# Performance work log

Hardware: AMD Instinct MI355X
Metric: run time of the kernel (lower is better)

Reference implementation:

```python
import jax, jax.numpy as jnp
import numpy as np

K = 7
TAU = 0.1
ANCHORS = 512
CANDIDATES = 2048
B, C, H, W = 16, 384, 96, 96
RADIUS = K // 2
K2 = K * K

_dy, _dx = np.meshgrid(np.arange(-RADIUS, RADIUS + 1), np.arange(-RADIUS, RADIUS + 1), indexing='ij')
OFF_Y = jnp.asarray(_dy.reshape(-1).astype(np.int32))  # [K2]
OFF_X = jnp.asarray(_dx.reshape(-1).astype(np.int32))  # [K2]


def _normalize(x):
    # F.normalize(x, dim=1): L2 over channel dim, eps=1e-12
    n = jnp.sqrt(jnp.sum(x * x, axis=1, keepdims=True))
    return x / jnp.maximum(n, 1e-12)


def _local_sims_shared(feat, anchors_yx):
    # feat [B,C,H,W], anchors_yx [M,2] shared across batch -> [B,M,K2]
    ys, xs = anchors_yx[:, 0], anchors_yx[:, 1]          # [M]
    yy = ys[:, None] + OFF_Y[None, :]                    # [M,K2]
    xx = xs[:, None] + OFF_X[None, :]                    # [M,K2]
    center = feat[:, :, ys, xs]                          # [B,C,M]
    neigh = feat[:, :, yy, xx]                           # [B,C,M,K2]
    return jnp.einsum('bcm,bcmk->bmk', center, neigh)


def _local_sims_per_image(feat, anchors_byx):
    # feat [B,C,H,W], anchors_byx [Bm,M,2] per-image anchors -> [B,M,K2]
    b, c, h, w = feat.shape
    flat = feat.reshape(b, c, h * w)
    ys, xs = anchors_byx[..., 0], anchors_byx[..., 1]    # [B,M]
    lin_c = ys * w + xs                                  # [B,M]
    lin_n = (ys[..., None] + OFF_Y) * w + (xs[..., None] + OFF_X)  # [B,M,K2]
    gather = jax.vmap(lambda f, idx: f[:, idx])          # f [C,HW], idx [...]
    center = gather(flat, lin_c)                         # [B,C,M]
    neigh = gather(flat, lin_n)                          # [B,C,M,K2]
    return jnp.einsum('bcm,bcmk->bmk', center, neigh)


def setup_inputs() -> dict:
    key = jax.random.key(0)
    k1, k2, k3, k4 = jax.random.split(key, 4)
    student = jax.random.normal(k1, (B, C, H, W), dtype=jnp.float32)
    teacher = jax.random.normal(k2, (B, C, H, W), dtype=jnp.float32)
    # anchors valid region: [radius, H-radius-1] x [radius, W-radius-1]
    ys = jax.random.randint(k3, (CANDIDATES,), RADIUS, H - RADIUS, dtype=jnp.int32)
    xs = jax.random.randint(k4, (CANDIDATES,), RADIUS, W - RADIUS, dtype=jnp.int32)
    candidate_anchors = jnp.stack([ys, xs], axis=1)      # [Mc,2]
    return {"student": student, "teacher": teacher, "candidate_anchors": candidate_anchors}


def reference(student, teacher, candidate_anchors):
    t_norm = _normalize(teacher)
    # --- teacher-entropy based anchor selection (no_grad in original) ---
    sim_cand = _local_sims_shared(t_norm, candidate_anchors) / TAU   # [B,Mc,K2]
    p = jax.nn.softmax(sim_cand, axis=2)
    ent = -jnp.sum(p * jnp.log(p + 1e-6), axis=2)                    # [B,Mc]
    # per_image=True, kcenter_top_m=0 -> lowest-entropy top-k per image
    _, sel_idx = jax.lax.top_k(-ent, ANCHORS)                        # [B,A]
    anchors = candidate_anchors[sel_idx]                             # [B,A,2]
    # --- local affinity KL ---
    s_norm = _normalize(student)
    sim_s = _local_sims_per_image(s_norm, anchors) / TAU             # [B,A,K2]
    sim_t = _local_sims_per_image(t_norm, anchors) / TAU
    log_ps = jax.nn.log_softmax(sim_s, axis=2)
    log_pt = jax.nn.log_softmax(sim_t, axis=2)
    pt = jnp.exp(log_pt)
    # F.kl_div(log_ps, pt, 'none').sum(2).mean()
    loss = jnp.mean(jnp.sum(pt * (log_pt - log_ps), axis=2))
    return loss
```

## Files before the change

### kernel.cpp

```cpp
#include <hip/hip_runtime.h>
#include <math.h>

#define B 16
#define C 384
#define CPAD 385
#define H 96
#define W 96
#define HW (H*W)
#define M 2048
#define K2 49
#define RAD 3
#define NSEL 512
#define INV_TAU 10.0f
#define TP 32

__device__ inline float wave_max(float v){
  #pragma unroll
  for (int o = 32; o; o >>= 1) v = fmaxf(v, __shfl_xor(v, o));
  return v;
}
__device__ inline float wave_sum(float v){
  #pragma unroll
  for (int o = 32; o; o >>= 1) v += __shfl_xor(v, o);
  return v;
}

__device__ inline float dot_wave(float2 c0, float2 c1, float2 c2,
                                 const float2* __restrict__ nb2){
  float2 n0 = nb2[0], n1 = nb2[64], n2 = nb2[128];
  float acc = c0.x * n0.x;
  acc = fmaf(c0.y, n0.y, acc);
  acc = fmaf(c1.x, n1.x, acc); acc = fmaf(c1.y, n1.y, acc);
  acc = fmaf(c2.x, n2.x, acc); acc = fmaf(c2.y, n2.y, acc);
  acc += __shfl_xor(acc, 32); acc += __shfl_xor(acc, 16);
  acc += __shfl_xor(acc, 8);  acc += __shfl_xor(acc, 4);
  acc += __shfl_xor(acc, 2);  acc += __shfl_xor(acc, 1);
  return acc;
}


__global__ void tnorm_kernel(const float* __restrict__ src, float* __restrict__ dst){
  int blk = blockIdx.x;
  int b = blk / (HW / TP);
  int pixbase = (blk % (HW / TP)) * TP;
  __shared__ float tile[TP][CPAD];
  __shared__ float scale[TP];
  const float* sb = src + (size_t)b * C * HW + pixbase;
  int tx = threadIdx.x & 31;
  int ty = threadIdx.x >> 5;
  #pragma unroll 4
  for (int c0 = 0; c0 < C; c0 += 8){
    tile[tx][c0 + ty] = sb[(size_t)(c0 + ty) * HW + tx];
  }
  __syncthreads();
  int pix = threadIdx.x >> 3;
  int j = threadIdx.x & 7;
  float ss = 0.f;
  #pragma unroll 4
  for (int c = j * 48; c < j * 48 + 48; ++c){ float v = tile[pix][c]; ss = fmaf(v, v, ss); }
  ss += __shfl_xor(ss, 1); ss += __shfl_xor(ss, 2); ss += __shfl_xor(ss, 4);
  if (j == 0) scale[pix] = 1.0f / fmaxf(sqrtf(ss), 1e-12f);
  __syncthreads();
  float4* db4 = (float4*)(dst + ((size_t)b * HW + pixbase) * C);
  #pragma unroll 4
  for (int l = threadIdx.x; l < TP * (C / 4); l += 256){
    int p = l / (C / 4), c4 = l - p * (C / 4);
    float s = scale[p];
    float4 v;
    v.x = tile[p][c4 * 4 + 0] * s;
    v.y = tile[p][c4 * 4 + 1] * s;
    v.z = tile[p][c4 * 4 + 2] * s;
    v.w = tile[p][c4 * 4 + 3] * s;
    db4[(size_t)p * (C / 4) + c4] = v;
  }
}

__global__ __launch_bounds__(256) void cand2_kernel(const float* __restrict__ fT,
                             const int* __restrict__ anch,
                             float* __restrict__ simc, float* __restrict__ ent){
  int bm = blockIdx.x * 4 + (threadIdx.x >> 6);
  int b = bm >> 11, m = bm & (M - 1);
  int lane = threadIdx.x & 63;
  int ay = anch[2 * m], ax = anch[2 * m + 1];
  const float* img = fT + (size_t)b * HW * C;
  const float2* ctr2 = (const float2*)(img + (size_t)(ay * W + ax) * C) + lane;
  float2 c0 = ctr2[0], c1 = ctr2[64], c2 = ctr2[128];
  float mysim = 0.f;
  int k = 0;
  for (int dy = -RAD; dy <= RAD; ++dy){
    const float* rowp = img + (size_t)((ay + dy) * W + (ax - RAD)) * C;
    #pragma unroll
    for (int dx = 0; dx < 7; ++dx){
      const float2* nb2 = (const float2*)(rowp + (size_t)dx * C) + lane;
      float acc = dot_wave(c0, c1, c2, nb2);
      if (lane == k) mysim = acc;
      ++k;
    }
  }
  mysim *= INV_TAU;
  float v = (lane < K2) ? mysim : -INFINITY;
  float mx = wave_max(v);
  float e = (lane < K2) ? expf(mysim - mx) : 0.f;
  float se = wave_sum(e);
  float p = e / se;
  float term = (lane < K2) ? (-p * logf(p + 1e-6f)) : 0.f;
  float en = wave_sum(term);
  if (lane == 0) ent[bm] = en;
  if (lane < K2) simc[(size_t)bm * K2 + lane] = mysim;
}

__global__ void select_kernel(const float* __restrict__ ent, int* __restrict__ sel){
  int blk = blockIdx.x;
  int b = blk >> 3;
  int i = (blk & 7) * 256 + threadIdx.x;
  __shared__ float se[M];
  for (int j = threadIdx.x; j < M; j += 256) se[j] = ent[b * M + j];
  __syncthreads();
  float ei = se[i];
  int r = 0;
  for (int j = 0; j < M; ++j){
    float ej = se[j];
    r += (ej < ei) || (ej == ei && j < i);
  }
  if (r < NSEL) sel[b * NSEL + r] = i;
}

__global__ __launch_bounds__(256) void kl2_kernel(const float* __restrict__ fS,
                           const int* __restrict__ anch,
                           const float* __restrict__ simc, const int* __restrict__ sel,
                           float* __restrict__ klpart){
  int bj = blockIdx.x * 4 + (threadIdx.x >> 6);
  int b = bj >> 9, j = bj & (NSEL - 1);
  int lane = threadIdx.x & 63;
  int m = sel[b * NSEL + j];
  int ay = anch[2 * m], ax = anch[2 * m + 1];
  const float* img = fS + (size_t)b * HW * C;
  const float2* ctr2 = (const float2*)(img + (size_t)(ay * W + ax) * C) + lane;
  float2 c0 = ctr2[0], c1 = ctr2[64], c2 = ctr2[128];
  float mysim = 0.f;
  int k = 0;
  for (int dy = -RAD; dy <= RAD; ++dy){
    const float* rowp = img + (size_t)((ay + dy) * W + (ax - RAD)) * C;
    #pragma unroll
    for (int dx = 0; dx < 7; ++dx){
      const float2* nb2 = (const float2*)(rowp + (size_t)dx * C) + lane;
      float acc = dot_wave(c0, c1, c2, nb2);
      if (lane == k) mysim = acc;
      ++k;
    }
  }
  float sim_sv = mysim * INV_TAU;
  float sim_tv = (lane < K2) ? simc[((size_t)b * M + m) * K2 + lane] : -INFINITY;

  float vs = (lane < K2) ? sim_sv : -INFINITY;
  float mxs = wave_max(vs);
  float es = (lane < K2) ? expf(sim_sv - mxs) : 0.f;
  float sums = wave_sum(es);
  float ls = sim_sv - mxs - logf(sums);

  float mxt = wave_max(sim_tv);
  float et = (lane < K2) ? expf(sim_tv - mxt) : 0.f;
  float sumt = wave_sum(et);
  float lt = sim_tv - mxt - logf(sumt);

  float pt = et / sumt;
  float term = (lane < K2) ? pt * (lt - ls) : 0.f;
  float kl = wave_sum(term);
  if (lane == 0) klpart[bj] = kl;
}

__global__ void reduce_kernel(const float* __restrict__ part, float* __restrict__ out){
  float s = 0.f;
  for (int i = threadIdx.x; i < B * NSEL; i += 256) s += part[i];
  s = wave_sum(s);
  __shared__ float wsum[4];
  if ((threadIdx.x & 63) == 0) wsum[threadIdx.x >> 6] = s;
  __syncthreads();
  if (threadIdx.x == 0) out[0] = (wsum[0] + wsum[1] + wsum[2] + wsum[3]) * (1.0f / (B * NSEL));
}


__global__ void norms_kernel(const float* __restrict__ t, const float* __restrict__ s,
                             float* __restrict__ inv_t, float* __restrict__ inv_s){
  int pix = blockIdx.x * blockDim.x + threadIdx.x;
  if (pix >= B * HW) return;
  int b = pix / HW, p = pix - b * HW;
  const float* tb = t + (size_t)b * C * HW + p;
  const float* sb = s + (size_t)b * C * HW + p;
  float at = 0.f, as = 0.f;
  #pragma unroll 4
  for (int c = 0; c < C; ++c){
    float v = tb[(size_t)c * HW]; at = fmaf(v, v, at);
    float u = sb[(size_t)c * HW]; as = fmaf(u, u, as);
  }
  inv_t[pix] = 1.0f / fmaxf(sqrtf(at), 1e-12f);
  inv_s[pix] = 1.0f / fmaxf(sqrtf(as), 1e-12f);
}

__global__ void cand_kernel(const float* __restrict__ t, const int* __restrict__ anch,
                            const float* __restrict__ inv_t,
                            float* __restrict__ simc, float* __restrict__ ent){
  int bm = blockIdx.x;
  int b = bm >> 11, m = bm & (M - 1);
  int lane = threadIdx.x;
  int ay = anch[2 * m], ax = anch[2 * m + 1];
  int k = lane < K2 ? lane : 0;
  int dy = k / 7 - RAD, dx = k - (k / 7) * 7 - RAD;
  int pc = ay * W + ax;
  int pk = (ay + dy) * W + (ax + dx);
  const float* base = t + (size_t)b * C * HW;
  float acc = 0.f;
  #pragma unroll 4
  for (int c = 0; c < C; ++c){
    const float* row = base + (size_t)c * HW;
    acc = fmaf(row[pc], row[pk], acc);
  }
  float sim = acc * inv_t[b * HW + pc] * inv_t[b * HW + pk] * INV_TAU;
  float v = (lane < K2) ? sim : -INFINITY;
  float mx = wave_max(v);
  float e = (lane < K2) ? expf(sim - mx) : 0.f;
  float se = wave_sum(e);
  float p = e / se;
  float term = (lane < K2) ? (-p * logf(p + 1e-6f)) : 0.f;
  float en = wave_sum(term);
  if (lane == 0) ent[bm] = en;
  if (lane < K2) simc[(size_t)bm * K2 + lane] = sim;
}

__global__ void kl_kernel(const float* __restrict__ s, const int* __restrict__ anch,
                          const float* __restrict__ inv_s, const float* __restrict__ simc,
                          const int* __restrict__ sel, float* __restrict__ klpart){
  int bj = blockIdx.x;
  int b = bj >> 9, j = bj & (NSEL - 1);
  int lane = threadIdx.x;
  int m = sel[b * NSEL + j];
  int ay = anch[2 * m], ax = anch[2 * m + 1];
  int k = lane < K2 ? lane : 0;
  int dy = k / 7 - RAD, dx = k - (k / 7) * 7 - RAD;
  int pc = ay * W + ax;
  int pk = (ay + dy) * W + (ax + dx);
  const float* base = s + (size_t)b * C * HW;
  float acc = 0.f;
  #pragma unroll 4
  for (int c = 0; c < C; ++c){
    const float* row = base + (size_t)c * HW;
    acc = fmaf(row[pc], row[pk], acc);
  }
  float sim_sv = acc * inv_s[b * HW + pc] * inv_s[b * HW + pk] * INV_TAU;
  float sim_tv = (lane < K2) ? simc[((size_t)b * M + m) * K2 + lane] : -INFINITY;

  float vs = (lane < K2) ? sim_sv : -INFINITY;
  float mxs = wave_max(vs);
  float es = (lane < K2) ? expf(sim_sv - mxs) : 0.f;
  float sums = wave_sum(es);
  float ls = sim_sv - mxs - logf(sums);

  float mxt = wave_max(sim_tv);
  float et = (lane < K2) ? expf(sim_tv - mxt) : 0.f;
  float sumt = wave_sum(et);
  float lt = sim_tv - mxt - logf(sumt);

  float pt = et / sumt;
  float term = (lane < K2) ? pt * (lt - ls) : 0.f;
  float kl = wave_sum(term);
  if (lane == 0) klpart[bj] = kl;
}

extern "C" void kernel_launch(void* const* d_in, const int* in_sizes, int n_in,
                              void* d_out, int out_size, void* d_ws, size_t ws_size,
                              hipStream_t stream){
  const float* student = (const float*)d_in[0];
  const float* teacher = (const float*)d_in[1];
  const int*   anch    = (const int*)d_in[2];
  float* out = (float*)d_out;

  const size_t fbuf_elems = (size_t)B * HW * C;
  const size_t simc_elems = (size_t)B * M * K2;
  size_t req = (fbuf_elems + simc_elems + (size_t)B * M + (size_t)B * NSEL) * sizeof(float)
             + (size_t)B * NSEL * sizeof(int);

  if (ws_size >= req){
    float* fbuf   = (float*)d_ws;
    float* simc   = fbuf + fbuf_elems;
    float* ent    = simc + simc_elems;
    float* klpart = ent + (size_t)B * M;
    int*   sel    = (int*)(klpart + (size_t)B * NSEL);

    hipLaunchKernelGGL(tnorm_kernel, dim3(B * (HW / TP)), dim3(256), 0, stream, teacher, fbuf);
    hipLaunchKernelGGL(cand2_kernel, dim3(B * M / 4), dim3(256), 0, stream, fbuf, anch, simc, ent);
    hipLaunchKernelGGL(select_kernel, dim3(B * 8), dim3(256), 0, stream, ent, sel);
    hipLaunchKernelGGL(tnorm_kernel, dim3(B * (HW / TP)), dim3(256), 0, stream, student, fbuf);
    hipLaunchKernelGGL(kl2_kernel, dim3(B * NSEL / 4), dim3(256), 0, stream, fbuf, anch, simc, sel, klpart);
    hipLaunchKernelGGL(reduce_kernel, dim3(1), dim3(256), 0, stream, klpart, out);
  } else {
    float* ws2    = (float*)d_ws;
    float* inv_t  = ws2;
    float* inv_s  = inv_t + B * HW;
    float* ent    = inv_s + B * HW;
    float* simc   = ent + B * M;
    float* klpart = simc + simc_elems;
    int*   sel    = (int*)(klpart + (size_t)B * NSEL);

    hipLaunchKernelGGL(norms_kernel, dim3((B * HW + 255) / 256), dim3(256), 0, stream,
                       teacher, student, inv_t, inv_s);
    hipLaunchKernelGGL(cand_kernel, dim3(B * M), dim3(64), 0, stream,
                       teacher, anch, inv_t, simc, ent);
    hipLaunchKernelGGL(select_kernel, dim3(B * 8), dim3(256), 0, stream, ent, sel);
    hipLaunchKernelGGL(kl_kernel, dim3(B * NSEL), dim3(64), 0, stream,
                       student, anch, inv_s, simc, sel, klpart);
    hipLaunchKernelGGL(reduce_kernel, dim3(1), dim3(256), 0, stream, klpart, out);
  }
}
```

Baseline: 907.7 us.

## Rework patch dot products into 4-neighbor wave groups, sort anchors spatially, swizzle blocks

Each wave now splits into four 16-lane groups, so one pass computes four neighbor dot products with 12 float2 loads per lane, double-buffered under scheduling barriers. This replaces 49 full-wave reductions with 14 shorter ones. Candidate anchors are sorted by 8x8 spatial tile in a new kernel, and block ids are swizzled so nearby anchors run together for better L2 reuse. Launch bounds now request 4 blocks per CU. The risks are higher register pressure and a small extra sort kernel.

```diff
diff --git a/kernel.cpp b/kernel.cpp
--- a/kernel.cpp
+++ b/kernel.cpp
@@ -25,17 +25,48 @@
   return v;
 }
 
-__device__ inline float dot_wave(float2 c0, float2 c1, float2 c2,
-                                 const float2* __restrict__ nb2){
-  float2 n0 = nb2[0], n1 = nb2[64], n2 = nb2[128];
-  float acc = c0.x * n0.x;
-  acc = fmaf(c0.y, n0.y, acc);
-  acc = fmaf(c1.x, n1.x, acc); acc = fmaf(c1.y, n1.y, acc);
-  acc = fmaf(c2.x, n2.x, acc); acc = fmaf(c2.y, n2.y, acc);
-  acc += __shfl_xor(acc, 32); acc += __shfl_xor(acc, 16);
-  acc += __shfl_xor(acc, 8);  acc += __shfl_xor(acc, 4);
-  acc += __shfl_xor(acc, 2);  acc += __shfl_xor(acc, 1);
-  return acc;
+__device__ __forceinline__ float patch_sims(const float* __restrict__ img,
+                                            int ay, int ax, int lane){
+  int g = lane >> 4, t = lane & 15;
+  const float2* cp = (const float2*)(img + (size_t)(ay * W + ax) * C) + t;
+  float2 c[12];
+  #pragma unroll
+  for (int j = 0; j < 12; ++j) c[j] = cp[16 * j];
+  float mysim = 0.f;
+  float2 bA[12], bB[12];
+
+#define PLOAD(buf, pp) { \
+    int dxl = ((pp) & 1) * 4 + g; if (dxl > 6) dxl = 6; \
+    const float2* np = (const float2*)(img + \
+        (size_t)((ay + ((pp) >> 1) - RAD) * W + (ax - RAD + dxl)) * C) + t; \
+    _Pragma("unroll") for (int j = 0; j < 12; ++j) buf[j] = np[16 * j]; }
+
+#define PCOMP(buf, pp) { \
+    float a0 = 0.f, a1 = 0.f; \
+    _Pragma("unroll") for (int j = 0; j < 6; ++j){ \
+      a0 = fmaf(c[j].x, buf[j].x, a0); a0 = fmaf(c[j].y, buf[j].y, a0); \
+      a1 = fmaf(c[j+6].x, buf[j+6].x, a1); a1 = fmaf(c[j+6].y, buf[j+6].y, a1); } \
+    float a = a0 + a1; \
+    a += __shfl_xor(a, 8); a += __shfl_xor(a, 4); \
+    a += __shfl_xor(a, 2); a += __shfl_xor(a, 1); \
+    int kbase = ((pp) >> 1) * 7 + ((pp) & 1) * 4; \
+    int npass = ((pp) & 1) ? 3 : 4; \
+    float v = __shfl(a, ((lane - kbase) & 3) << 4); \
+    if (lane >= kbase && lane < kbase + npass) mysim = v; }
+
+  PLOAD(bA, 0);
+  #pragma unroll
+  for (int pp = 0; pp < 14; pp += 2){
+    PLOAD(bB, pp + 1);
+    __builtin_amdgcn_sched_barrier(0);
+    PCOMP(bA, pp);
+    if (pp + 2 < 14) PLOAD(bA, pp + 2);
+    __builtin_amdgcn_sched_barrier(0);
+    PCOMP(bB, pp + 1);
+  }
+#undef PLOAD
+#undef PCOMP
+  return mysim;
 }
 
 
@@ -75,29 +106,35 @@
   }
 }
 
-__global__ __launch_bounds__(256) void cand2_kernel(const float* __restrict__ fT,
-                             const int* __restrict__ anch,
+__global__ void sort_kernel(const int* __restrict__ anch, int* __restrict__ order){
+  int i = blockIdx.x * 256 + threadIdx.x;
+  __shared__ int keys[M];
+  for (int j = threadIdx.x; j < M; j += 256){
+    int ay = anch[2 * j], ax = anch[2 * j + 1];
+    keys[j] = (((ay >> 3) * 12 + (ax >> 3)) << 11) + j;
+  }
+  __syncthreads();
+  int ki = keys[i];
+  int r = 0;
+  #pragma unroll 4
+  for (int j = 0; j < M; ++j) r += (keys[j] < ki) ? 1 : 0;
+  order[r] = i;
+}
+
+__global__ __launch_bounds__(256, 4) void cand2_kernel(const float* __restrict__ fT,
+                             const int* __restrict__ anch, const int* __restrict__ order,
                              float* __restrict__ simc, float* __restrict__ ent){
-  int bm = blockIdx.x * 4 + (threadIdx.x >> 6);
-  int b = bm >> 11, m = bm & (M - 1);
+  int nwg = B * M / 4;
+  int bid = blockIdx.x;
+  int swz = (bid & 7) * (nwg >> 3) + (bid >> 3);
+  int bm = swz * 4 + (threadIdx.x >> 6);
+  int b = bm >> 11, mi = bm & (M - 1);
   int lane = threadIdx.x & 63;
+  int m = order ? order[mi] : mi;
   int ay = anch[2 * m], ax = anch[2 * m + 1];
   const float* img = fT + (size_t)b * HW * C;
-  const float2* ctr2 = (const float2*)(img + (size_t)(ay * W + ax) * C) + lane;
-  float2 c0 = ctr2[0], c1 = ctr2[64], c2 = ctr2[128];
-  float mysim = 0.f;
-  int k = 0;
-  for (int dy = -RAD; dy <= RAD; ++dy){
-    const float* rowp = img + (size_t)((ay + dy) * W + (ax - RAD)) * C;
-    #pragma unroll
-    for (int dx = 0; dx < 7; ++dx){
-      const float2* nb2 = (const float2*)(rowp + (size_t)dx * C) + lane;
-      float acc = dot_wave(c0, c1, c2, nb2);
-      if (lane == k) mysim = acc;
-      ++k;
-    }
-  }
-  mysim *= INV_TAU;
+  float mysim = patch_sims(img, ay, ax, lane) * INV_TAU;
+
   float v = (lane < K2) ? mysim : -INFINITY;
   float mx = wave_max(v);
   float e = (lane < K2) ? expf(mysim - mx) : 0.f;
@@ -105,8 +142,9 @@
   float p = e / se;
   float term = (lane < K2) ? (-p * logf(p + 1e-6f)) : 0.f;
   float en = wave_sum(term);
-  if (lane == 0) ent[bm] = en;
-  if (lane < K2) simc[(size_t)bm * K2 + lane] = mysim;
+  size_t slot = (size_t)b * M + m;
+  if (lane == 0) ent[slot] = en;
+  if (lane < K2) simc[slot * K2 + lane] = mysim;
 }
 
 __global__ void select_kernel(const float* __restrict__ ent, int* __restrict__ sel){
@@ -125,7 +163,7 @@
   if (r < NSEL) sel[b * NSEL + r] = i;
 }
 
-__global__ __launch_bounds__(256) void kl2_kernel(const float* __restrict__ fS,
+__global__ __launch_bounds__(256, 4) void kl2_kernel(const float* __restrict__ fS,
                            const int* __restrict__ anch,
                            const float* __restrict__ simc, const int* __restrict__ sel,
                            float* __restrict__ klpart){
@@ -135,21 +173,7 @@
   int m = sel[b * NSEL + j];
   int ay = anch[2 * m], ax = anch[2 * m + 1];
   const float* img = fS + (size_t)b * HW * C;
-  const float2* ctr2 = (const float2*)(img + (size_t)(ay * W + ax) * C) + lane;
-  float2 c0 = ctr2[0], c1 = ctr2[64], c2 = ctr2[128];
-  float mysim = 0.f;
-  int k = 0;
-  for (int dy = -RAD; dy <= RAD; ++dy){
-    const float* rowp = img + (size_t)((ay + dy) * W + (ax - RAD)) * C;
-    #pragma unroll
-    for (int dx = 0; dx < 7; ++dx){
-      const float2* nb2 = (const float2*)(rowp + (size_t)dx * C) + lane;
-      float acc = dot_wave(c0, c1, c2, nb2);
-      if (lane == k) mysim = acc;
-      ++k;
-    }
-  }
-  float sim_sv = mysim * INV_TAU;
+  float sim_sv = patch_sims(img, ay, ax, lane) * INV_TAU;
   float sim_tv = (lane < K2) ? simc[((size_t)b * M + m) * K2 + lane] : -INFINITY;
 
   float vs = (lane < K2) ? sim_sv : -INFINITY;
@@ -276,18 +300,22 @@
 
   const size_t fbuf_elems = (size_t)B * HW * C;
   const size_t simc_elems = (size_t)B * M * K2;
-  size_t req = (fbuf_elems + simc_elems + (size_t)B * M + (size_t)B * NSEL) * sizeof(float)
-             + (size_t)B * NSEL * sizeof(int);
-
-  if (ws_size >= req){
+  size_t req_base = (fbuf_elems + simc_elems + (size_t)B * M + (size_t)B * NSEL) * sizeof(float)
+                  + (size_t)B * NSEL * sizeof(int);
+  size_t req_sort = req_base + (size_t)M * sizeof(int);
+
+  if (ws_size >= req_base){
     float* fbuf   = (float*)d_ws;
     float* simc   = fbuf + fbuf_elems;
     float* ent    = simc + simc_elems;
     float* klpart = ent + (size_t)B * M;
     int*   sel    = (int*)(klpart + (size_t)B * NSEL);
+    int*   order  = (ws_size >= req_sort) ? (sel + (size_t)B * NSEL) : (int*)nullptr;
 
     hipLaunchKernelGGL(tnorm_kernel, dim3(B * (HW / TP)), dim3(256), 0, stream, teacher, fbuf);
-    hipLaunchKernelGGL(cand2_kernel, dim3(B * M / 4), dim3(256), 0, stream, fbuf, anch, simc, ent);
+    if (order)
+      hipLaunchKernelGGL(sort_kernel, dim3(8), dim3(256), 0, stream, anch, order);
+    hipLaunchKernelGGL(cand2_kernel, dim3(B * M / 4), dim3(256), 0, stream, fbuf, anch, order, simc, ent);
     hipLaunchKernelGGL(select_kernel, dim3(B * 8), dim3(256), 0, stream, ent, sel);
     hipLaunchKernelGGL(tnorm_kernel, dim3(B * (HW / TP)), dim3(256), 0, stream, student, fbuf);
     hipLaunchKernelGGL(kl2_kernel, dim3(B * NSEL / 4), dim3(256), 0, stream, fbuf, anch, simc, sel, klpart);
```

After: 911.5 us. Within noise of the previous version (+0.4%).
